# Kernel optimization log

Hardware: AMD Instinct MI355X
Metric: run time of the kernel (lower is better)

The kernel has to match this reference:

```python
import jax, jax.numpy as jnp
import numpy as np

N_NODES = 100000


def _add_self_loops(edge_index, n):
    loop = jnp.arange(n, dtype=edge_index.dtype)
    src = jnp.concatenate([edge_index[0], loop])
    dst = jnp.concatenate([edge_index[1], loop])
    return src, dst


def _gcn_conv(x, src, dst, n, W, b):
    # PyG GCNConv: h = x W; symmetric normalization with self-loops; scatter-add; + bias
    h = x @ W                                   # [N, out]
    ones = jnp.ones(src.shape[0], dtype=x.dtype)
    deg = jax.ops.segment_sum(ones, dst, num_segments=n)   # in-degree incl. self-loop
    dinv = jax.lax.rsqrt(deg)                   # deg >= 1 because of self-loops
    norm = dinv[src] * dinv[dst]                # [E]
    msg = h[src] * norm[:, None]                # gather + scale  [E, out]
    out = jax.ops.segment_sum(msg, dst, num_segments=n)     # scatter-add
    return out + b


def setup_inputs() -> dict:
    key = jax.random.key(0)
    k1, k2, k3, k4, k5 = jax.random.split(key, 5)
    n, e = N_NODES, 1600000
    d_in, d_hid, d_out = 128, 128, 40
    x = jax.random.normal(k1, (n, d_in), dtype=jnp.float32)
    edge_index = jax.random.randint(k2, (2, e), 0, n, dtype=jnp.int32)
    s = 1.0 / np.sqrt(d_in)
    W1 = jax.random.uniform(k3, (d_in, d_hid), jnp.float32, -s, s)
    b1 = jnp.zeros((d_hid,), jnp.float32)
    s2 = 1.0 / np.sqrt(d_hid)
    W2 = jax.random.uniform(k4, (d_hid, d_hid), jnp.float32, -s2, s2)
    b2 = jnp.zeros((d_hid,), jnp.float32)
    Wout = jax.random.uniform(k5, (d_hid, d_out), jnp.float32, -s2, s2)
    bout = jnp.zeros((d_out,), jnp.float32)
    return {"x": x, "edge_index": edge_index, "W1": W1, "b1": b1,
            "W2": W2, "b2": b2, "Wout": Wout, "bout": bout}


def reference(x, edge_index, W1, b1, W2, b2, Wout, bout):
    n = x.shape[0]
    src, dst = _add_self_loops(edge_index, n)
    h = _gcn_conv(x, src, dst, n, W1, b1)
    h = jax.nn.relu(h)
    # dropout(p=0.6) is identity in eval mode
    h = _gcn_conv(h, src, dst, n, W2, b2)
    return h @ Wout + bout
```

## Files before the change

### kernel.cpp

```cpp
#include <hip/hip_runtime.h>


typedef __attribute__((ext_vector_type(8))) short short8;
typedef __attribute__((ext_vector_type(4))) float floatx4;
typedef __attribute__((ext_vector_type(2))) float floatx2;
typedef _Float16 f16;
typedef __attribute__((ext_vector_type(4))) _Float16 half4;

#define CSR_STRIDE 64
#define CH 4096
#define BCAP2 10240

static __device__ inline unsigned short f32_to_bf16(float f) {
    unsigned u = __float_as_uint(f);
    unsigned r = (u + 0x7FFFu + ((u >> 16) & 1u)) >> 16;
    return (unsigned short)r;
}
static __device__ inline float bf16_to_f32(unsigned short h) {
    return __uint_as_float(((unsigned)h) << 16);
}
static __device__ inline void split2(float v, unsigned short& h, unsigned short& l) {
    h = f32_to_bf16(v);
    l = f32_to_bf16(v - bf16_to_f32(h));
}
static __device__ __forceinline__ void fp8x8_acc(floatx2* s2, uint2 v) {
    s2[0] += __builtin_amdgcn_cvt_pk_f32_fp8(v.x, false);
    s2[1] += __builtin_amdgcn_cvt_pk_f32_fp8(v.x, true);
    s2[2] += __builtin_amdgcn_cvt_pk_f32_fp8(v.y, false);
    s2[3] += __builtin_amdgcn_cvt_pk_f32_fp8(v.y, true);
}


__global__ __launch_bounds__(256) void bin_scatter(const int* __restrict__ src,
                                                   const int* __restrict__ dst,
                                                   int* __restrict__ bcur,
                                                   unsigned* __restrict__ bstore, int e) {
    __shared__ int hist[256];
    __shared__ int gbase[256];
    __shared__ int curs[256];
    int t = threadIdx.x;
    hist[t] = 0;
    __syncthreads();
    int tot4 = e >> 2;
    int base4 = blockIdx.x * (CH / 4);
    unsigned pay[16];
    int cbv[16];
    bool vg[4];
    #pragma unroll
    for (int j = 0; j < 4; j++) {
        int i4 = base4 + t + 256 * j;
        vg[j] = (i4 < tot4);
        if (vg[j]) {
            int4 s4 = ((const int4*)src)[i4];
            int4 d4 = ((const int4*)dst)[i4];
            int dd[4] = {d4.x, d4.y, d4.z, d4.w};
            int ss[4] = {s4.x, s4.y, s4.z, s4.w};
            #pragma unroll
            for (int q = 0; q < 4; q++) {
                int cb = dd[q] >> 9;
                cbv[j * 4 + q] = cb;
                pay[j * 4 + q] = (unsigned)ss[q] | ((unsigned)(dd[q] & 511) << 17);
                atomicAdd(&hist[cb], 1);
            }
        }
    }
    __syncthreads();
    gbase[t] = atomicAdd(&bcur[t * 16], hist[t]);
    curs[t] = 0;
    __syncthreads();
    #pragma unroll
    for (int j = 0; j < 4; j++) {
        if (vg[j]) {
            #pragma unroll
            for (int q = 0; q < 4; q++) {
                int b = cbv[j * 4 + q];
                int pos = atomicAdd(&curs[b], 1);
                int o = gbase[b] + pos;
                if (o < BCAP2) bstore[(size_t)b * BCAP2 + o] = pay[j * 4 + q];
            }
        }
    }
}


__global__ __launch_bounds__(1024) void bin_to_csr(const int* __restrict__ bcur,
                                                   const unsigned* __restrict__ bstore,
                                                   int* __restrict__ csr,
                                                   int* __restrict__ cnt,
                                                   float* __restrict__ dinv, int n) {
    __shared__ int lcur[512];
    int b = blockIdx.x;
    int t = threadIdx.x;
    if (t < 512) lcur[t] = 0;
    __syncthreads();
    int cb = bcur[b * 16];
    if (cb > BCAP2) cb = BCAP2;
    const unsigned* bs = bstore + (size_t)b * BCAP2;
    for (int i = t; i < cb; i += 1024) {
        unsigned v = bs[i];
        int dl = v >> 17;
        int pos = atomicAdd(&lcur[dl], 1);
        if (pos < CSR_STRIDE) {
            int node = (b << 9) | dl;
            csr[(size_t)node * CSR_STRIDE + pos] = (int)(v & 0x1FFFFu);
        }
    }
    __syncthreads();
    if (t < 512) {
        int node = (b << 9) + t;
        if (node < n) {
            int c = min(lcur[t], CSR_STRIDE);
            cnt[node] = c;
            dinv[node] = rsqrtf((float)c + 1.0f);
            int end = (c + 7) & ~7;
            if (end < 8) end = 8;
            size_t base = (size_t)node * CSR_STRIDE;
            for (int k = c; k < end; k++) csr[base + k] = n;
        }
    }
}


__global__ __launch_bounds__(256) void wc_build(const float* __restrict__ W2,
                                                const float* __restrict__ Wout,
                                                const float* __restrict__ b2,
                                                const float* __restrict__ bout,
                                                float* __restrict__ Wc,
                                                float* __restrict__ bc) {
    int tid = blockIdx.x * 256 + threadIdx.x;
    if (tid < 5120) {
        int i = tid / 40, j = tid - (tid / 40) * 40;
        float s = 0.f;
        for (int k = 0; k < 128; k++) s = fmaf(W2[i * 128 + k], Wout[k * 40 + j], s);
        Wc[i * 40 + j] = s;
    } else if (tid < 5160) {
        int j = tid - 5120;
        float s = bout[j];
        for (int k = 0; k < 128; k++) s = fmaf(b2[k], Wout[k * 40 + j], s);
        bc[j] = s;
    }
}


__global__ __launch_bounds__(256) void wsplit_kernel(const float* __restrict__ W1,
                                                     const float* __restrict__ Wcf,
                                                     unsigned short* __restrict__ wf1,
                                                     unsigned short* __restrict__ wfc) {
    int idx = blockIdx.x * 256 + threadIdx.x;
    if (idx < 16384) {
        int e = idx;
        int k = e >> 7, nn = e & 127;
        unsigned short h, l;
        split2(W1[e], h, l);
        int c = nn >> 4, s = k >> 5;
        int lane = (nn & 15) | (((k >> 3) & 3) << 4);
        int j = k & 7;
        int o = ((c * 4 + s) * 64 + lane) * 8 + j;
        wf1[o] = h;
        wf1[16384 + o] = l;
    } else if (idx < 16384 + 6144) {
        int id = idx - 16384;
        int j = id & 7, lane = (id >> 3) & 63, cs = id >> 9;
        int c = cs >> 2, s = cs & 3;
        int k = s * 32 + ((lane >> 4) & 3) * 8 + j;
        int nn = c * 16 + (lane & 15);
        float v = (nn < 40) ? Wcf[k * 40 + nn] : 0.f;
        unsigned short h, l;
        split2(v, h, l);
        wfc[id] = h;
        wfc[6144 + id] = l;
    }
}


__global__ __launch_bounds__(256, 2) void gemm_mfma(const float* __restrict__ A,
                                                    const unsigned short* __restrict__ Wf,
                                                    const float* __restrict__ dinv,
                                                    unsigned char* __restrict__ ht, int M) {
    __shared__ __align__(16) unsigned short Wl[32768];
    {
        const float4* wsrc = (const float4*)Wf;
        float4* wdst = (float4*)Wl;
        #pragma unroll
        for (int i = 0; i < 16; i++) wdst[threadIdx.x + 256 * i] = wsrc[threadIdx.x + 256 * i];
    }
    int wave = threadIdx.x >> 6, lane = threadIdx.x & 63;
    int mlo = lane & 15, kq = lane >> 4;
    int row_base = blockIdx.x * 128 + wave * 32;

    short8 a[2][4][2];
    #pragma unroll
    for (int rt = 0; rt < 2; rt++) {
        int row = row_base + rt * 16 + mlo;
        if (row > M - 1) row = M - 1;
        const float* pa = A + (size_t)row * 128 + kq * 8;
        #pragma unroll
        for (int s = 0; s < 4; s++) {
            float u[8];
            *(float4*)&u[0] = *(const float4*)(pa + s * 32);
            *(float4*)&u[4] = *(const float4*)(pa + s * 32 + 4);
            short8 ah, al;
            #pragma unroll
            for (int j = 0; j < 8; j++) {
                unsigned short h, l;
                split2(u[j], h, l);
                ah[j] = (short)h;
                al[j] = (short)l;
            }
            a[rt][s][0] = ah;
            a[rt][s][1] = al;
        }
    }
    floatx4 acc[2][8];
    #pragma unroll
    for (int rt = 0; rt < 2; rt++)
        #pragma unroll
        for (int c = 0; c < 8; c++) acc[rt][c] = (floatx4){0.f, 0.f, 0.f, 0.f};
    __syncthreads();

    #pragma unroll
    for (int c = 0; c < 8; c++) {
        #pragma unroll
        for (int s = 0; s < 4; s++) {
            int fo = ((c * 4 + s) * 64 + lane) * 8;
            short8 bhi = *(const short8*)&Wl[fo];
            short8 blo = *(const short8*)&Wl[16384 + fo];
            #pragma unroll
            for (int rt = 0; rt < 2; rt++) {
                acc[rt][c] = __builtin_amdgcn_mfma_f32_16x16x32_bf16(a[rt][s][0], bhi, acc[rt][c], 0, 0, 0);
                acc[rt][c] = __builtin_amdgcn_mfma_f32_16x16x32_bf16(a[rt][s][1], bhi, acc[rt][c], 0, 0, 0);
                acc[rt][c] = __builtin_amdgcn_mfma_f32_16x16x32_bf16(a[rt][s][0], blo, acc[rt][c], 0, 0, 0);
            }
        }
    }
    #pragma unroll
    for (int rt = 0; rt < 2; rt++) {
        int r0 = row_base + rt * 16 + kq * 4;
        #pragma unroll
        for (int r = 0; r < 4; r++) {
            int row = r0 + r;
            if (row >= M) continue;
            float dd = dinv[row];
            unsigned char* hp = ht + (size_t)row * 128 + mlo;
            #pragma unroll
            for (int c = 0; c < 8; c++) {
                float v = acc[rt][c][r] * dd;
                unsigned pk = __builtin_amdgcn_cvt_pk_fp8_f32(v, v, 0u, false);
                hp[c * 16] = (unsigned char)(pk & 0xFFu);
            }
        }
    }
}


__device__ __forceinline__ void gather16_fp8_to_lds(const unsigned char* __restrict__ ht,
                                                    const int* __restrict__ cnt,
                                                    const int* __restrict__ csr,
                                                    const float* __restrict__ dinv,
                                                    const float* __restrict__ bias,
                                                    int n, unsigned short* __restrict__ ldsA) {
    int g = threadIdx.x >> 4;
    int l = threadIdx.x & 15;
    int d = blockIdx.x * 16 + g;
    if (d >= n) return;
    const unsigned char* hb = ht + l * 8;
    const int4* c4 = (const int4*)(csr + (size_t)d * CSR_STRIDE);
    int4 ea0 = c4[0], ea1 = c4[1];
    int4 eb0 = c4[2], eb1 = c4[3];
    uint2 sv = *(const uint2*)(hb + (size_t)d * 128);
    int len = cnt[d];
    uint2 p0 = *(const uint2*)(hb + (size_t)ea0.x * 128);
    uint2 p1 = *(const uint2*)(hb + (size_t)ea0.y * 128);
    uint2 p2 = *(const uint2*)(hb + (size_t)ea0.z * 128);
    uint2 p3 = *(const uint2*)(hb + (size_t)ea0.w * 128);
    uint2 p4 = *(const uint2*)(hb + (size_t)ea1.x * 128);
    uint2 p5 = *(const uint2*)(hb + (size_t)ea1.y * 128);
    uint2 p6 = *(const uint2*)(hb + (size_t)ea1.z * 128);
    uint2 p7 = *(const uint2*)(hb + (size_t)ea1.w * 128);
    floatx2 s2[4];
    #pragma unroll
    for (int j = 0; j < 4; j++) s2[j] = (floatx2){0.f, 0.f};
    fp8x8_acc(s2, sv);
    int lenp = (len + 7) & ~7;
    if (lenp < 8) lenp = 8;
    for (int it = 8; it < lenp; it += 8) {
        int qidx = (it >> 2) + 2;
        int i0 = qidx > 14 ? 14 : qidx;
        int i1 = qidx + 1 > 15 ? 15 : qidx + 1;
        int4 ec0 = c4[i0];
        int4 ec1 = c4[i1];
        uint2 q0 = *(const uint2*)(hb + (size_t)eb0.x * 128);
        uint2 q1 = *(const uint2*)(hb + (size_t)eb0.y * 128);
        uint2 q2 = *(const uint2*)(hb + (size_t)eb0.z * 128);
        uint2 q3 = *(const uint2*)(hb + (size_t)eb0.w * 128);
        uint2 q4 = *(const uint2*)(hb + (size_t)eb1.x * 128);
        uint2 q5 = *(const uint2*)(hb + (size_t)eb1.y * 128);
        uint2 q6 = *(const uint2*)(hb + (size_t)eb1.z * 128);
        uint2 q7 = *(const uint2*)(hb + (size_t)eb1.w * 128);
        fp8x8_acc(s2, p0); fp8x8_acc(s2, p1); fp8x8_acc(s2, p2); fp8x8_acc(s2, p3);
        fp8x8_acc(s2, p4); fp8x8_acc(s2, p5); fp8x8_acc(s2, p6); fp8x8_acc(s2, p7);
        p0 = q0; p1 = q1; p2 = q2; p3 = q3;
        p4 = q4; p5 = q5; p6 = q6; p7 = q7;
        eb0 = ec0; eb1 = ec1;
    }
    fp8x8_acc(s2, p0); fp8x8_acc(s2, p1); fp8x8_acc(s2, p2); fp8x8_acc(s2, p3);
    fp8x8_acc(s2, p4); fp8x8_acc(s2, p5); fp8x8_acc(s2, p6); fp8x8_acc(s2, p7);
    float dd = dinv[d];
    const float4* b4 = (const float4*)bias;
    float4 ba = b4[l * 2 + 0];
    float4 bq = b4[l * 2 + 1];
    float o[8];
    o[0] = fmaf(s2[0][0], dd, ba.x);
    o[1] = fmaf(s2[0][1], dd, ba.y);
    o[2] = fmaf(s2[1][0], dd, ba.z);
    o[3] = fmaf(s2[1][1], dd, ba.w);
    o[4] = fmaf(s2[2][0], dd, bq.x);
    o[5] = fmaf(s2[2][1], dd, bq.y);
    o[6] = fmaf(s2[3][0], dd, bq.z);
    o[7] = fmaf(s2[3][1], dd, bq.w);
    short8 h8, l8;
    #pragma unroll
    for (int j = 0; j < 8; j++) {
        float v = fmaxf(o[j], 0.f);
        unsigned short sh, sl;
        split2(v, sh, sl);
        h8[j] = (short)sh;
        l8[j] = (short)sl;
    }
    *(short8*)&ldsA[g * 136 + l * 8] = h8;
    *(short8*)&ldsA[2176 + g * 136 + l * 8] = l8;
}

__device__ __forceinline__ void lds_afrag16(const unsigned short* __restrict__ ldsA,
                                            short8 ah[4], short8 al[4]) {
    int lane = threadIdx.x & 63;
    int m = lane & 15, kq = lane >> 4;
    #pragma unroll
    for (int s = 0; s < 4; s++) {
        int c = 4 * s + kq;
        ah[s] = *(const short8*)&ldsA[m * 136 + c * 8];
        al[s] = *(const short8*)&ldsA[2176 + m * 136 + c * 8];
    }
}

__global__ __launch_bounds__(256) void gather_gemm_hidden(const unsigned char* __restrict__ ht,
                                                          const int* __restrict__ cnt,
                                                          const int* __restrict__ csr,
                                                          const float* __restrict__ dinv,
                                                          const float* __restrict__ bias,
                                                          const unsigned short* __restrict__ Wf,
                                                          f16* __restrict__ z, int n) {
    __shared__ __align__(16) unsigned short ldsA[4352];
    gather16_fp8_to_lds(ht, cnt, csr, dinv, bias, n, ldsA);
    __syncthreads();
    int wave = threadIdx.x >> 6, lane = threadIdx.x & 63;
    if (wave == 3) {
        int row = blockIdx.x * 16 + (lane >> 2);
        if (row < n) {
            uint2 zz; zz.x = 0u; zz.y = 0u;
            *(uint2*)(z + (size_t)row * 64 + 48 + (lane & 3) * 4) = zz;
        }
        return;
    }
    short8 ah[4], al[4];
    lds_afrag16(ldsA, ah, al);
    int m = lane & 15, kq = lane >> 4;
    int c = wave;
    floatx4 acc = (floatx4){0.f, 0.f, 0.f, 0.f};
    #pragma unroll
    for (int s = 0; s < 4; s++) {
        int fo = ((c * 4 + s) * 64 + lane) * 8;
        short8 bhi = *(const short8*)&Wf[fo];
        short8 blo = *(const short8*)&Wf[6144 + fo];
        acc = __builtin_amdgcn_mfma_f32_16x16x32_bf16(ah[s], bhi, acc, 0, 0, 0);
        acc = __builtin_amdgcn_mfma_f32_16x16x32_bf16(al[s], bhi, acc, 0, 0, 0);
        acc = __builtin_amdgcn_mfma_f32_16x16x32_bf16(ah[s], blo, acc, 0, 0, 0);
    }
    #pragma unroll
    for (int r = 0; r < 4; r++) {
        int row = blockIdx.x * 16 + kq * 4 + r;
        if (row < n) z[(size_t)row * 64 + c * 16 + m] = (f16)(acc[r] * dinv[row]);
    }
}

#define H4ACC(P) { s0 += (float)P[0]; s1 += (float)P[1]; s2 += (float)P[2]; s3 += (float)P[3]; }

__global__ __launch_bounds__(256) void gather_out(const f16* __restrict__ z,
                                                  const int* __restrict__ cnt,
                                                  const int* __restrict__ csr,
                                                  const float* __restrict__ dinv,
                                                  const float* __restrict__ bc,
                                                  float* __restrict__ out, int n) {
    int g = threadIdx.x >> 4;
    int l = threadIdx.x & 15;
    int d = blockIdx.x * 16 + g;
    if (d >= n) return;
    const f16* zb = z + l * 4;
    const int4* c4 = (const int4*)(csr + (size_t)d * CSR_STRIDE);
    int4 ea0 = c4[0], ea1 = c4[1];
    int4 eb0 = c4[2], eb1 = c4[3];
    half4 sv = *(const half4*)(zb + (size_t)d * 64);
    int len = cnt[d];
    half4 p0 = *(const half4*)(zb + (size_t)ea0.x * 64);
    half4 p1 = *(const half4*)(zb + (size_t)ea0.y * 64);
    half4 p2 = *(const half4*)(zb + (size_t)ea0.z * 64);
    half4 p3 = *(const half4*)(zb + (size_t)ea0.w * 64);
    half4 p4 = *(const half4*)(zb + (size_t)ea1.x * 64);
    half4 p5 = *(const half4*)(zb + (size_t)ea1.y * 64);
    half4 p6 = *(const half4*)(zb + (size_t)ea1.z * 64);
    half4 p7 = *(const half4*)(zb + (size_t)ea1.w * 64);
    float s0 = (float)sv[0], s1 = (float)sv[1], s2 = (float)sv[2], s3 = (float)sv[3];
    int lenp = (len + 7) & ~7;
    if (lenp < 8) lenp = 8;
    for (int it = 8; it < lenp; it += 8) {
        int qidx = (it >> 2) + 2;
        int i0 = qidx > 14 ? 14 : qidx;
        int i1 = qidx + 1 > 15 ? 15 : qidx + 1;
        int4 ec0 = c4[i0];
        int4 ec1 = c4[i1];
        half4 q0 = *(const half4*)(zb + (size_t)eb0.x * 64);
        half4 q1 = *(const half4*)(zb + (size_t)eb0.y * 64);
        half4 q2 = *(const half4*)(zb + (size_t)eb0.z * 64);
        half4 q3 = *(const half4*)(zb + (size_t)eb0.w * 64);
        half4 q4 = *(const half4*)(zb + (size_t)eb1.x * 64);
        half4 q5 = *(const half4*)(zb + (size_t)eb1.y * 64);
        half4 q6 = *(const half4*)(zb + (size_t)eb1.z * 64);
        half4 q7 = *(const half4*)(zb + (size_t)eb1.w * 64);
        H4ACC(p0); H4ACC(p1); H4ACC(p2); H4ACC(p3);
        H4ACC(p4); H4ACC(p5); H4ACC(p6); H4ACC(p7);
        p0 = q0; p1 = q1; p2 = q2; p3 = q3;
        p4 = q4; p5 = q5; p6 = q6; p7 = q7;
        eb0 = ec0; eb1 = ec1;
    }
    H4ACC(p0); H4ACC(p1); H4ACC(p2); H4ACC(p3);
    H4ACC(p4); H4ACC(p5); H4ACC(p6); H4ACC(p7);
    if (l < 10) {
        float dd = dinv[d];
        float4 bb = ((const float4*)bc)[l];
        float4 o;
        o.x = fmaf(s0, dd, bb.x);
        o.y = fmaf(s1, dd, bb.y);
        o.z = fmaf(s2, dd, bb.z);
        o.w = fmaf(s3, dd, bb.w);
        *(float4*)(out + (size_t)d * 40 + l * 4) = o;
    }
}

extern "C" void kernel_launch(void* const* d_in, const int* in_sizes, int n_in,
                              void* d_out, int out_size, void* d_ws, size_t ws_size,
                              hipStream_t stream) {
    const float* x    = (const float*)d_in[0];
    const int*   ei   = (const int*)d_in[1];
    const float* W1   = (const float*)d_in[2];
    const float* b1   = (const float*)d_in[3];
    const float* W2   = (const float*)d_in[4];
    const float* b2   = (const float*)d_in[5];
    const float* Wout = (const float*)d_in[6];
    const float* bout = (const float*)d_in[7];

    int N = in_sizes[0] / 128;
    int E = in_sizes[1] / 2;
    const int* srcv = ei;
    const int* dstv = ei + E;

    char* p = (char*)d_ws;
    auto alloc = [&](size_t bytes) { void* r = (void*)p; p += (bytes + 255) & ~(size_t)255; return r; };
    int*      bcur   = (int*)alloc(256 * 16 * 4);
    int*      cnt    = (int*)alloc((size_t)N * 4);
    float*    dinv   = (float*)alloc((size_t)N * 4);
    unsigned* bstore = (unsigned*)alloc((size_t)256 * BCAP2 * 4);
    int*      csr    = (int*)alloc((size_t)N * CSR_STRIDE * 4);
    unsigned short* wf1 = (unsigned short*)alloc(32768 * 2);
    unsigned short* wfc = (unsigned short*)alloc(12288 * 2);
    float*    Wcf    = (float*)alloc(5120 * 4);
    float*    bc     = (float*)alloc(40 * 4);
    unsigned char* ht = (unsigned char*)alloc((size_t)(N + 1) * 128);
    f16*      z      = (f16*)alloc((size_t)(N + 1) * 64 * 2);

    int NB_A  = (E + CH - 1) / CH;
    int NB_B  = (N + 511) >> 9;
    int NB_G  = (N + 127) / 128;
    int NB_GG = (N + 15) / 16;

    wc_build<<<21, 256, 0, stream>>>(W2, Wout, b2, bout, Wcf, bc);
    wsplit_kernel<<<88, 256, 0, stream>>>(W1, Wcf, wf1, wfc);
    hipMemsetAsync(bcur, 0, 256 * 16 * 4, stream);
    hipMemsetAsync(ht + (size_t)N * 128, 0, 128, stream);
    hipMemsetAsync(z + (size_t)N * 64, 0, 128, stream);

    bin_scatter<<<NB_A, 256, 0, stream>>>(srcv, dstv, bcur, bstore, E);
    bin_to_csr<<<NB_B, 1024, 0, stream>>>(bcur, bstore, csr, cnt, dinv, N);
    gemm_mfma<<<NB_G, 256, 0, stream>>>(x, wf1, dinv, ht, N);

    gather_gemm_hidden<<<NB_GG, 256, 0, stream>>>(ht, cnt, csr, dinv, b1, wfc, z, N);
    gather_out<<<NB_GG, 256, 0, stream>>>(z, cnt, csr, dinv, bc, (float*)d_out, N);
}
```

Measured before the change: 225.0 us.

## Process two destination nodes per thread group in gather kernels

Both gather kernels now give each 16-lane group two destination nodes, interleaving their neighbor loads so twice as many independent memory requests are in flight per thread. Block count halves and the hidden-layer GEMM runs two 16-row MFMA tiles per block. Nodes with shorter edge lists are padded with loads of the zeroed sentinel row. This adds wasted loads when degrees differ, raises register pressure, and doubles LDS use.

```diff
diff --git a/kernel.cpp b/kernel.cpp
--- a/kernel.cpp
+++ b/kernel.cpp
@@ -253,7 +253,7 @@
 }
 
 
-__device__ __forceinline__ void gather16_fp8_to_lds(const unsigned char* __restrict__ ht,
+__device__ __forceinline__ void gather32_fp8_to_lds(const unsigned char* __restrict__ ht,
                                                     const int* __restrict__ cnt,
                                                     const int* __restrict__ csr,
                                                     const float* __restrict__ dinv,
@@ -261,85 +261,113 @@
                                                     int n, unsigned short* __restrict__ ldsA) {
     int g = threadIdx.x >> 4;
     int l = threadIdx.x & 15;
-    int d = blockIdx.x * 16 + g;
-    if (d >= n) return;
+    int dA = blockIdx.x * 32 + g;
+    int dB = dA + 16;
+    int eA = dA < n ? dA : 0;
+    int eB = dB < n ? dB : 0;
     const unsigned char* hb = ht + l * 8;
-    const int4* c4 = (const int4*)(csr + (size_t)d * CSR_STRIDE);
-    int4 ea0 = c4[0], ea1 = c4[1];
-    int4 eb0 = c4[2], eb1 = c4[3];
-    uint2 sv = *(const uint2*)(hb + (size_t)d * 128);
-    int len = cnt[d];
-    uint2 p0 = *(const uint2*)(hb + (size_t)ea0.x * 128);
-    uint2 p1 = *(const uint2*)(hb + (size_t)ea0.y * 128);
-    uint2 p2 = *(const uint2*)(hb + (size_t)ea0.z * 128);
-    uint2 p3 = *(const uint2*)(hb + (size_t)ea0.w * 128);
-    uint2 p4 = *(const uint2*)(hb + (size_t)ea1.x * 128);
-    uint2 p5 = *(const uint2*)(hb + (size_t)ea1.y * 128);
-    uint2 p6 = *(const uint2*)(hb + (size_t)ea1.z * 128);
-    uint2 p7 = *(const uint2*)(hb + (size_t)ea1.w * 128);
-    floatx2 s2[4];
-    #pragma unroll
-    for (int j = 0; j < 4; j++) s2[j] = (floatx2){0.f, 0.f};
-    fp8x8_acc(s2, sv);
-    int lenp = (len + 7) & ~7;
-    if (lenp < 8) lenp = 8;
-    for (int it = 8; it < lenp; it += 8) {
+    const int4* cA = (const int4*)(csr + (size_t)eA * CSR_STRIDE);
+    const int4* cB = (const int4*)(csr + (size_t)eB * CSR_STRIDE);
+    int4 a0 = cA[0], a1 = cA[1], b0 = cB[0], b1 = cB[1];
+    int4 na0 = cA[2], na1 = cA[3], nb0 = cB[2], nb1 = cB[3];
+    uint2 svA = *(const uint2*)(hb + (size_t)eA * 128);
+    uint2 svB = *(const uint2*)(hb + (size_t)eB * 128);
+    int lenA = cnt[eA], lenB = cnt[eB];
+    uint2 pA0 = *(const uint2*)(hb + (size_t)a0.x * 128);
+    uint2 pA1 = *(const uint2*)(hb + (size_t)a0.y * 128);
+    uint2 pA2 = *(const uint2*)(hb + (size_t)a0.z * 128);
+    uint2 pA3 = *(const uint2*)(hb + (size_t)a0.w * 128);
+    uint2 pA4 = *(const uint2*)(hb + (size_t)a1.x * 128);
+    uint2 pA5 = *(const uint2*)(hb + (size_t)a1.y * 128);
+    uint2 pA6 = *(const uint2*)(hb + (size_t)a1.z * 128);
+    uint2 pA7 = *(const uint2*)(hb + (size_t)a1.w * 128);
+    uint2 pB0 = *(const uint2*)(hb + (size_t)b0.x * 128);
+    uint2 pB1 = *(const uint2*)(hb + (size_t)b0.y * 128);
+    uint2 pB2 = *(const uint2*)(hb + (size_t)b0.z * 128);
+    uint2 pB3 = *(const uint2*)(hb + (size_t)b0.w * 128);
+    uint2 pB4 = *(const uint2*)(hb + (size_t)b1.x * 128);
+    uint2 pB5 = *(const uint2*)(hb + (size_t)b1.y * 128);
+    uint2 pB6 = *(const uint2*)(hb + (size_t)b1.z * 128);
+    uint2 pB7 = *(const uint2*)(hb + (size_t)b1.w * 128);
+    floatx2 sA[4], sB[4];
+    #pragma unroll
+    for (int j = 0; j < 4; j++) { sA[j] = (floatx2){0.f, 0.f}; sB[j] = (floatx2){0.f, 0.f}; }
+    fp8x8_acc(sA, svA);
+    fp8x8_acc(sB, svB);
+    int lenpA = (lenA + 7) & ~7; if (lenpA < 8) lenpA = 8;
+    int lenpB = (lenB + 7) & ~7; if (lenpB < 8) lenpB = 8;
+    int maxL = lenpA > lenpB ? lenpA : lenpB;
+    for (int it = 8; it < maxL; it += 8) {
         int qidx = (it >> 2) + 2;
         int i0 = qidx > 14 ? 14 : qidx;
         int i1 = qidx + 1 > 15 ? 15 : qidx + 1;
-        int4 ec0 = c4[i0];
-        int4 ec1 = c4[i1];
-        uint2 q0 = *(const uint2*)(hb + (size_t)eb0.x * 128);
-        uint2 q1 = *(const uint2*)(hb + (size_t)eb0.y * 128);
-        uint2 q2 = *(const uint2*)(hb + (size_t)eb0.z * 128);
-        uint2 q3 = *(const uint2*)(hb + (size_t)eb0.w * 128);
-        uint2 q4 = *(const uint2*)(hb + (size_t)eb1.x * 128);
-        uint2 q5 = *(const uint2*)(hb + (size_t)eb1.y * 128);
-        uint2 q6 = *(const uint2*)(hb + (size_t)eb1.z * 128);
-        uint2 q7 = *(const uint2*)(hb + (size_t)eb1.w * 128);
-        fp8x8_acc(s2, p0); fp8x8_acc(s2, p1); fp8x8_acc(s2, p2); fp8x8_acc(s2, p3);
-        fp8x8_acc(s2, p4); fp8x8_acc(s2, p5); fp8x8_acc(s2, p6); fp8x8_acc(s2, p7);
-        p0 = q0; p1 = q1; p2 = q2; p3 = q3;
-        p4 = q4; p5 = q5; p6 = q6; p7 = q7;
-        eb0 = ec0; eb1 = ec1;
-    }
-    fp8x8_acc(s2, p0); fp8x8_acc(s2, p1); fp8x8_acc(s2, p2); fp8x8_acc(s2, p3);
-    fp8x8_acc(s2, p4); fp8x8_acc(s2, p5); fp8x8_acc(s2, p6); fp8x8_acc(s2, p7);
-    float dd = dinv[d];
+        int4 ma0 = cA[i0], ma1 = cA[i1];
+        int4 mb0 = cB[i0], mb1 = cB[i1];
+        bool vA = it < lenpA, vB = it < lenpB;
+        int ax = vA ? na0.x : n, ay = vA ? na0.y : n, az = vA ? na0.z : n, aw = vA ? na0.w : n;
+        int ex = vA ? na1.x : n, ey = vA ? na1.y : n, ez = vA ? na1.z : n, ew = vA ? na1.w : n;
+        int bx = vB ? nb0.x : n, by = vB ? nb0.y : n, bz = vB ? nb0.z : n, bw = vB ? nb0.w : n;
+        int fx = vB ? nb1.x : n, fy = vB ? nb1.y : n, fz = vB ? nb1.z : n, fw = vB ? nb1.w : n;
+        uint2 qA0 = *(const uint2*)(hb + (size_t)ax * 128);
+        uint2 qA1 = *(const uint2*)(hb + (size_t)ay * 128);
+        uint2 qA2 = *(const uint2*)(hb + (size_t)az * 128);
+        uint2 qA3 = *(const uint2*)(hb + (size_t)aw * 128);
+        uint2 qA4 = *(const uint2*)(hb + (size_t)ex * 128);
+        uint2 qA5 = *(const uint2*)(hb + (size_t)ey * 128);
+        uint2 qA6 = *(const uint2*)(hb + (size_t)ez * 128);
+        uint2 qA7 = *(const uint2*)(hb + (size_t)ew * 128);
+        uint2 qB0 = *(const uint2*)(hb + (size_t)bx * 128);
+        uint2 qB1 = *(const uint2*)(hb + (size_t)by * 128);
+        uint2 qB2 = *(const uint2*)(hb + (size_t)bz * 128);
+        uint2 qB3 = *(const uint2*)(hb + (size_t)bw * 128);
+        uint2 qB4 = *(const uint2*)(hb + (size_t)fx * 128);
+        uint2 qB5 = *(const uint2*)(hb + (size_t)fy * 128);
+        uint2 qB6 = *(const uint2*)(hb + (size_t)fz * 128);
+        uint2 qB7 = *(const uint2*)(hb + (size_t)fw * 128);
+        fp8x8_acc(sA, pA0); fp8x8_acc(sA, pA1); fp8x8_acc(sA, pA2); fp8x8_acc(sA, pA3);
+        fp8x8_acc(sA, pA4); fp8x8_acc(sA, pA5); fp8x8_acc(sA, pA6); fp8x8_acc(sA, pA7);
+        fp8x8_acc(sB, pB0); fp8x8_acc(sB, pB1); fp8x8_acc(sB, pB2); fp8x8_acc(sB, pB3);
+        fp8x8_acc(sB, pB4); fp8x8_acc(sB, pB5); fp8x8_acc(sB, pB6); fp8x8_acc(sB, pB7);
+        pA0 = qA0; pA1 = qA1; pA2 = qA2; pA3 = qA3;
+        pA4 = qA4; pA5 = qA5; pA6 = qA6; pA7 = qA7;
+        pB0 = qB0; pB1 = qB1; pB2 = qB2; pB3 = qB3;
+        pB4 = qB4; pB5 = qB5; pB6 = qB6; pB7 = qB7;
+        na0 = ma0; na1 = ma1; nb0 = mb0; nb1 = mb1;
+    }
+    fp8x8_acc(sA, pA0); fp8x8_acc(sA, pA1); fp8x8_acc(sA, pA2); fp8x8_acc(sA, pA3);
+    fp8x8_acc(sA, pA4); fp8x8_acc(sA, pA5); fp8x8_acc(sA, pA6); fp8x8_acc(sA, pA7);
+    fp8x8_acc(sB, pB0); fp8x8_acc(sB, pB1); fp8x8_acc(sB, pB2); fp8x8_acc(sB, pB3);
+    fp8x8_acc(sB, pB4); fp8x8_acc(sB, pB5); fp8x8_acc(sB, pB6); fp8x8_acc(sB, pB7);
     const float4* b4 = (const float4*)bias;
     float4 ba = b4[l * 2 + 0];
     float4 bq = b4[l * 2 + 1];
-    float o[8];
-    o[0] = fmaf(s2[0][0], dd, ba.x);
-    o[1] = fmaf(s2[0][1], dd, ba.y);
-    o[2] = fmaf(s2[1][0], dd, ba.z);
-    o[3] = fmaf(s2[1][1], dd, ba.w);
-    o[4] = fmaf(s2[2][0], dd, bq.x);
-    o[5] = fmaf(s2[2][1], dd, bq.y);
-    o[6] = fmaf(s2[3][0], dd, bq.z);
-    o[7] = fmaf(s2[3][1], dd, bq.w);
-    short8 h8, l8;
-    #pragma unroll
-    for (int j = 0; j < 8; j++) {
-        float v = fmaxf(o[j], 0.f);
-        unsigned short sh, sl;
-        split2(v, sh, sl);
-        h8[j] = (short)sh;
-        l8[j] = (short)sl;
-    }
-    *(short8*)&ldsA[g * 136 + l * 8] = h8;
-    *(short8*)&ldsA[2176 + g * 136 + l * 8] = l8;
-}
-
-__device__ __forceinline__ void lds_afrag16(const unsigned short* __restrict__ ldsA,
-                                            short8 ah[4], short8 al[4]) {
-    int lane = threadIdx.x & 63;
-    int m = lane & 15, kq = lane >> 4;
-    #pragma unroll
-    for (int s = 0; s < 4; s++) {
-        int c = 4 * s + kq;
-        ah[s] = *(const short8*)&ldsA[m * 136 + c * 8];
-        al[s] = *(const short8*)&ldsA[2176 + m * 136 + c * 8];
+    #pragma unroll
+    for (int half = 0; half < 2; half++) {
+        int d = half ? dB : dA;
+        if (d >= n) continue;
+        floatx2* s2 = half ? sB : sA;
+        float dd = dinv[d];
+        float o[8];
+        o[0] = fmaf(s2[0][0], dd, ba.x);
+        o[1] = fmaf(s2[0][1], dd, ba.y);
+        o[2] = fmaf(s2[1][0], dd, ba.z);
+        o[3] = fmaf(s2[1][1], dd, ba.w);
+        o[4] = fmaf(s2[2][0], dd, bq.x);
+        o[5] = fmaf(s2[2][1], dd, bq.y);
+        o[6] = fmaf(s2[3][0], dd, bq.z);
+        o[7] = fmaf(s2[3][1], dd, bq.w);
+        short8 h8, l8;
+        #pragma unroll
+        for (int j = 0; j < 8; j++) {
+            float v = fmaxf(o[j], 0.f);
+            unsigned short sh, sl;
+            split2(v, sh, sl);
+            h8[j] = (short)sh;
+            l8[j] = (short)sl;
+        }
+        int row = g + half * 16;
+        *(short8*)&ldsA[row * 136 + l * 8] = h8;
+        *(short8*)&ldsA[4352 + row * 136 + l * 8] = l8;
     }
 }
 
@@ -350,40 +378,49 @@
                                                           const float* __restrict__ bias,
                                                           const unsigned short* __restrict__ Wf,
                                                           f16* __restrict__ z, int n) {
-    __shared__ __align__(16) unsigned short ldsA[4352];
-    gather16_fp8_to_lds(ht, cnt, csr, dinv, bias, n, ldsA);
+    __shared__ __align__(16) unsigned short ldsA[8704];
+    gather32_fp8_to_lds(ht, cnt, csr, dinv, bias, n, ldsA);
     __syncthreads();
     int wave = threadIdx.x >> 6, lane = threadIdx.x & 63;
     if (wave == 3) {
-        int row = blockIdx.x * 16 + (lane >> 2);
+        int row = blockIdx.x * 32 + (lane >> 1);
+        int chunk = lane & 1;
         if (row < n) {
-            uint2 zz; zz.x = 0u; zz.y = 0u;
-            *(uint2*)(z + (size_t)row * 64 + 48 + (lane & 3) * 4) = zz;
+            int4 zz; zz.x = 0; zz.y = 0; zz.z = 0; zz.w = 0;
+            *(int4*)(z + (size_t)row * 64 + 48 + chunk * 8) = zz;
         }
         return;
     }
-    short8 ah[4], al[4];
-    lds_afrag16(ldsA, ah, al);
     int m = lane & 15, kq = lane >> 4;
     int c = wave;
-    floatx4 acc = (floatx4){0.f, 0.f, 0.f, 0.f};
-    #pragma unroll
-    for (int s = 0; s < 4; s++) {
-        int fo = ((c * 4 + s) * 64 + lane) * 8;
-        short8 bhi = *(const short8*)&Wf[fo];
-        short8 blo = *(const short8*)&Wf[6144 + fo];
-        acc = __builtin_amdgcn_mfma_f32_16x16x32_bf16(ah[s], bhi, acc, 0, 0, 0);
-        acc = __builtin_amdgcn_mfma_f32_16x16x32_bf16(al[s], bhi, acc, 0, 0, 0);
-        acc = __builtin_amdgcn_mfma_f32_16x16x32_bf16(ah[s], blo, acc, 0, 0, 0);
-    }
-    #pragma unroll
-    for (int r = 0; r < 4; r++) {
-        int row = blockIdx.x * 16 + kq * 4 + r;
-        if (row < n) z[(size_t)row * 64 + c * 16 + m] = (f16)(acc[r] * dinv[row]);
-    }
-}
-
-#define H4ACC(P) { s0 += (float)P[0]; s1 += (float)P[1]; s2 += (float)P[2]; s3 += (float)P[3]; }
+    #pragma unroll
+    for (int rt = 0; rt < 2; rt++) {
+        short8 ah[4], al[4];
+        #pragma unroll
+        for (int s = 0; s < 4; s++) {
+            int cc = 4 * s + kq;
+            ah[s] = *(const short8*)&ldsA[(rt * 16 + m) * 136 + cc * 8];
+            al[s] = *(const short8*)&ldsA[4352 + (rt * 16 + m) * 136 + cc * 8];
+        }
+        floatx4 acc = (floatx4){0.f, 0.f, 0.f, 0.f};
+        #pragma unroll
+        for (int s = 0; s < 4; s++) {
+            int fo = ((c * 4 + s) * 64 + lane) * 8;
+            short8 bhi = *(const short8*)&Wf[fo];
+            short8 blo = *(const short8*)&Wf[6144 + fo];
+            acc = __builtin_amdgcn_mfma_f32_16x16x32_bf16(ah[s], bhi, acc, 0, 0, 0);
+            acc = __builtin_amdgcn_mfma_f32_16x16x32_bf16(al[s], bhi, acc, 0, 0, 0);
+            acc = __builtin_amdgcn_mfma_f32_16x16x32_bf16(ah[s], blo, acc, 0, 0, 0);
+        }
+        #pragma unroll
+        for (int r = 0; r < 4; r++) {
+            int row = blockIdx.x * 32 + rt * 16 + kq * 4 + r;
+            if (row < n) z[(size_t)row * 64 + c * 16 + m] = (f16)(acc[r] * dinv[row]);
+        }
+    }
+}
+
+#define H4ACC(S, P) { S##0 += (float)P[0]; S##1 += (float)P[1]; S##2 += (float)P[2]; S##3 += (float)P[3]; }
 
 __global__ __launch_bounds__(256) void gather_out(const f16* __restrict__ z,
                                                   const int* __restrict__ cnt,
@@ -393,56 +430,100 @@
                                                   float* __restrict__ out, int n) {
     int g = threadIdx.x >> 4;
     int l = threadIdx.x & 15;
-    int d = blockIdx.x * 16 + g;
-    if (d >= n) return;
+    int dA = blockIdx.x * 32 + g;
+    int dB = dA + 16;
+    int eA = dA < n ? dA : 0;
+    int eB = dB < n ? dB : 0;
     const f16* zb = z + l * 4;
-    const int4* c4 = (const int4*)(csr + (size_t)d * CSR_STRIDE);
-    int4 ea0 = c4[0], ea1 = c4[1];
-    int4 eb0 = c4[2], eb1 = c4[3];
-    half4 sv = *(const half4*)(zb + (size_t)d * 64);
-    int len = cnt[d];
-    half4 p0 = *(const half4*)(zb + (size_t)ea0.x * 64);
-    half4 p1 = *(const half4*)(zb + (size_t)ea0.y * 64);
-    half4 p2 = *(const half4*)(zb + (size_t)ea0.z * 64);
-    half4 p3 = *(const half4*)(zb + (size_t)ea0.w * 64);
-    half4 p4 = *(const half4*)(zb + (size_t)ea1.x * 64);
-    half4 p5 = *(const half4*)(zb + (size_t)ea1.y * 64);
-    half4 p6 = *(const half4*)(zb + (size_t)ea1.z * 64);
-    half4 p7 = *(const half4*)(zb + (size_t)ea1.w * 64);
-    float s0 = (float)sv[0], s1 = (float)sv[1], s2 = (float)sv[2], s3 = (float)sv[3];
-    int lenp = (len + 7) & ~7;
-    if (lenp < 8) lenp = 8;
-    for (int it = 8; it < lenp; it += 8) {
+    const int4* cA = (const int4*)(csr + (size_t)eA * CSR_STRIDE);
+    const int4* cB = (const int4*)(csr + (size_t)eB * CSR_STRIDE);
+    int4 a0 = cA[0], a1 = cA[1], b0 = cB[0], b1 = cB[1];
+    int4 na0 = cA[2], na1 = cA[3], nb0 = cB[2], nb1 = cB[3];
+    half4 svA = *(const half4*)(zb + (size_t)eA * 64);
+    half4 svB = *(const half4*)(zb + (size_t)eB * 64);
+    int lenA = cnt[eA], lenB = cnt[eB];
+    half4 pA0 = *(const half4*)(zb + (size_t)a0.x * 64);
+    half4 pA1 = *(const half4*)(zb + (size_t)a0.y * 64);
+    half4 pA2 = *(const half4*)(zb + (size_t)a0.z * 64);
+    half4 pA3 = *(const half4*)(zb + (size_t)a0.w * 64);
+    half4 pA4 = *(const half4*)(zb + (size_t)a1.x * 64);
+    half4 pA5 = *(const half4*)(zb + (size_t)a1.y * 64);
+    half4 pA6 = *(const half4*)(zb + (size_t)a1.z * 64);
+    half4 pA7 = *(const half4*)(zb + (size_t)a1.w * 64);
+    half4 pB0 = *(const half4*)(zb + (size_t)b0.x * 64);
+    half4 pB1 = *(const half4*)(zb + (size_t)b0.y * 64);
+    half4 pB2 = *(const half4*)(zb + (size_t)b0.z * 64);
+    half4 pB3 = *(const half4*)(zb + (size_t)b0.w * 64);
+    half4 pB4 = *(const half4*)(zb + (size_t)b1.x * 64);
+    half4 pB5 = *(const half4*)(zb + (size_t)b1.y * 64);
+    half4 pB6 = *(const half4*)(zb + (size_t)b1.z * 64);
+    half4 pB7 = *(const half4*)(zb + (size_t)b1.w * 64);
+    float sA0 = (float)svA[0], sA1 = (float)svA[1], sA2 = (float)svA[2], sA3 = (float)svA[3];
+    float sB0 = (float)svB[0], sB1 = (float)svB[1], sB2 = (float)svB[2], sB3 = (float)svB[3];
+    int lenpA = (lenA + 7) & ~7; if (lenpA < 8) lenpA = 8;
+    int lenpB = (lenB + 7) & ~7; if (lenpB < 8) lenpB = 8;
+    int maxL = lenpA > lenpB ? lenpA : lenpB;
+    for (int it = 8; it < maxL; it += 8) {
         int qidx = (it >> 2) + 2;
         int i0 = qidx > 14 ? 14 : qidx;
         int i1 = qidx + 1 > 15 ? 15 : qidx + 1;
-        int4 ec0 = c4[i0];
-        int4 ec1 = c4[i1];
-        half4 q0 = *(const half4*)(zb + (size_t)eb0.x * 64);
-        half4 q1 = *(const half4*)(zb + (size_t)eb0.y * 64);
-        half4 q2 = *(const half4*)(zb + (size_t)eb0.z * 64);
-        half4 q3 = *(const half4*)(zb + (size_t)eb0.w * 64);
-        half4 q4 = *(const half4*)(zb + (size_t)eb1.x * 64);
-        half4 q5 = *(const half4*)(zb + (size_t)eb1.y * 64);
-        half4 q6 = *(const half4*)(zb + (size_t)eb1.z * 64);
-        half4 q7 = *(const half4*)(zb + (size_t)eb1.w * 64);
-        H4ACC(p0); H4ACC(p1); H4ACC(p2); H4ACC(p3);
-        H4ACC(p4); H4ACC(p5); H4ACC(p6); H4ACC(p7);
-        p0 = q0; p1 = q1; p2 = q2; p3 = q3;
-        p4 = q4; p5 = q5; p6 = q6; p7 = q7;
-        eb0 = ec0; eb1 = ec1;
-    }
-    H4ACC(p0); H4ACC(p1); H4ACC(p2); H4ACC(p3);
-    H4ACC(p4); H4ACC(p5); H4ACC(p6); H4ACC(p7);
+        int4 ma0 = cA[i0], ma1 = cA[i1];
+        int4 mb0 = cB[i0], mb1 = cB[i1];
+        bool vA = it < lenpA, vB = it < lenpB;
+        int ax = vA ? na0.x : n, ay = vA ? na0.y : n, az = vA ? na0.z : n, aw = vA ? na0.w : n;
+        int ex = vA ? na1.x : n, ey = vA ? na1.y : n, ez = vA ? na1.z : n, ew = vA ? na1.w : n;
+        int bx = vB ? nb0.x : n, by = vB ? nb0.y : n, bz = vB ? nb0.z : n, bw = vB ? nb0.w : n;
+        int fx = vB ? nb1.x : n, fy = vB ? nb1.y : n, fz = vB ? nb1.z : n, fw = vB ? nb1.w : n;
+        half4 qA0 = *(const half4*)(zb + (size_t)ax * 64);
+        half4 qA1 = *(const half4*)(zb + (size_t)ay * 64);
+        half4 qA2 = *(const half4*)(zb + (size_t)az * 64);
+        half4 qA3 = *(const half4*)(zb + (size_t)aw * 64);
+        half4 qA4 = *(const half4*)(zb + (size_t)ex * 64);
+        half4 qA5 = *(const half4*)(zb + (size_t)ey * 64);
+        half4 qA6 = *(const half4*)(zb + (size_t)ez * 64);
+        half4 qA7 = *(const half4*)(zb + (size_t)ew * 64);
+        half4 qB0 = *(const half4*)(zb + (size_t)bx * 64);
+        half4 qB1 = *(const half4*)(zb + (size_t)by * 64);
+        half4 qB2 = *(const half4*)(zb + (size_t)bz * 64);
+        half4 qB3 = *(const half4*)(zb + (size_t)bw * 64);
+        half4 qB4 = *(const half4*)(zb + (size_t)fx * 64);
+        half4 qB5 = *(const half4*)(zb + (size_t)fy * 64);
+        half4 qB6 = *(const half4*)(zb + (size_t)fz * 64);
+        half4 qB7 = *(const half4*)(zb + (size_t)fw * 64);
+        H4ACC(sA, pA0); H4ACC(sA, pA1); H4ACC(sA, pA2); H4ACC(sA, pA3);
+        H4ACC(sA, pA4); H4ACC(sA, pA5); H4ACC(sA, pA6); H4ACC(sA, pA7);
+        H4ACC(sB, pB0); H4ACC(sB, pB1); H4ACC(sB, pB2); H4ACC(sB, pB3);
+        H4ACC(sB, pB4); H4ACC(sB, pB5); H4ACC(sB, pB6); H4ACC(sB, pB7);
+        pA0 = qA0; pA1 = qA1; pA2 = qA2; pA3 = qA3;
+        pA4 = qA4; pA5 = qA5; pA6 = qA6; pA7 = qA7;
+        pB0 = qB0; pB1 = qB1; pB2 = qB2; pB3 = qB3;
+        pB4 = qB4; pB5 = qB5; pB6 = qB6; pB7 = qB7;
+        na0 = ma0; na1 = ma1; nb0 = mb0; nb1 = mb1;
+    }
+    H4ACC(sA, pA0); H4ACC(sA, pA1); H4ACC(sA, pA2); H4ACC(sA, pA3);
+    H4ACC(sA, pA4); H4ACC(sA, pA5); H4ACC(sA, pA6); H4ACC(sA, pA7);
+    H4ACC(sB, pB0); H4ACC(sB, pB1); H4ACC(sB, pB2); H4ACC(sB, pB3);
+    H4ACC(sB, pB4); H4ACC(sB, pB5); H4ACC(sB, pB6); H4ACC(sB, pB7);
     if (l < 10) {
-        float dd = dinv[d];
         float4 bb = ((const float4*)bc)[l];
-        float4 o;
-        o.x = fmaf(s0, dd, bb.x);
-        o.y = fmaf(s1, dd, bb.y);
-        o.z = fmaf(s2, dd, bb.z);
-        o.w = fmaf(s3, dd, bb.w);
-        *(float4*)(out + (size_t)d * 40 + l * 4) = o;
+        if (dA < n) {
+            float dd = dinv[dA];
+            float4 o;
+            o.x = fmaf(sA0, dd, bb.x);
+            o.y = fmaf(sA1, dd, bb.y);
+            o.z = fmaf(sA2, dd, bb.z);
+            o.w = fmaf(sA3, dd, bb.w);
+            *(float4*)(out + (size_t)dA * 40 + l * 4) = o;
+        }
+        if (dB < n) {
+            float dd = dinv[dB];
+            float4 o;
+            o.x = fmaf(sB0, dd, bb.x);
+            o.y = fmaf(sB1, dd, bb.y);
+            o.z = fmaf(sB2, dd, bb.z);
+            o.w = fmaf(sB3, dd, bb.w);
+            *(float4*)(out + (size_t)dB * 40 + l * 4) = o;
+        }
     }
 }
 
@@ -480,7 +561,7 @@
     int NB_A  = (E + CH - 1) / CH;
     int NB_B  = (N + 511) >> 9;
     int NB_G  = (N + 127) / 128;
-    int NB_GG = (N + 15) / 16;
+    int NB_GG = (N + 31) / 32;
 
     wc_build<<<21, 256, 0, stream>>>(W2, Wout, b2, bout, Wcf, bc);
     wsplit_kernel<<<88, 256, 0, stream>>>(W1, Wcf, wf1, wfc);
```

After: 235.1 us. 4.5% more time.
